# Kernel optimization log

Measured on AMD Instinct MI355X. Metric: run time of the kernel, lower is better.

## Reference

```python
import jax, jax.numpy as jnp
import numpy as np

IN_FEATURES = 4096
OUT_FEATURES = 4096
BINS = 65536
TOKENS = 8192


def setup_inputs() -> dict:
    key = jax.random.key(0)
    k_x, k_w, k_b, k_idx = jax.random.split(key, 4)
    bound = 1.0 / np.sqrt(OUT_FEATURES)
    x = jax.random.normal(k_x, (TOKENS, IN_FEATURES), dtype=jnp.float32)
    weight = jax.random.uniform(k_w, (BINS,), dtype=jnp.float32, minval=-bound, maxval=bound)
    bias = jax.random.uniform(k_b, (OUT_FEATURES,), dtype=jnp.float32, minval=-bound, maxval=bound)
    indices_hash = jax.random.randint(k_idx, (OUT_FEATURES * IN_FEATURES,), 0, BINS, dtype=jnp.int32)
    return {"x": x, "weight": weight, "bias": bias, "indices_hash": indices_hash}


def reference(x, weight, bias, indices_hash):
    # Reconstruct dense weight [out, in] by gathering from the shared bins.
    true_weight = jnp.take(weight, indices_hash, axis=0).reshape(OUT_FEATURES, IN_FEATURES)
    # F.linear: x @ W^T + b
    return jnp.einsum("ti,oi->to", x, true_weight) + bias
```

## Files before the change

kernel.cpp:

```cpp
#include <hip/hip_runtime.h>
#include <hip/hip_bf16.h>

#define TOKENS 8192
#define NOUT   4096
#define KIN    4096

typedef __attribute__((ext_vector_type(8))) short short8;
typedef __attribute__((ext_vector_type(4))) float f32x4;

__device__ __forceinline__ short f2bf(float f) {
  union { float f; unsigned u; } v; v.f = f;
  unsigned r = v.u + 0x7fffu + ((v.u >> 16) & 1u);
  return (short)(r >> 16);
}

__device__ __forceinline__ void async_copy16(const void* g, void* l) {
  __builtin_amdgcn_global_load_lds(
      (const __attribute__((address_space(1))) void*)g,
      (__attribute__((address_space(3))) void*)l, 16, 0, 0);
}

__global__ void pack_w_kernel(const int4* __restrict__ idx,
                              const float* __restrict__ w,
                              short8* __restrict__ wb) {
  size_t t = (size_t)blockIdx.x * blockDim.x + threadIdx.x;
  int4 a = idx[2 * t];
  int4 b = idx[2 * t + 1];
  short8 o;
  o[0] = f2bf(w[a.x]); o[1] = f2bf(w[a.y]);
  o[2] = f2bf(w[a.z]); o[3] = f2bf(w[a.w]);
  o[4] = f2bf(w[b.x]); o[5] = f2bf(w[b.y]);
  o[6] = f2bf(w[b.z]); o[7] = f2bf(w[b.w]);
  wb[t] = o;
}

__global__ void pack_x_kernel(const float4* __restrict__ x,
                              short8* __restrict__ xb) {
  size_t t = (size_t)blockIdx.x * blockDim.x + threadIdx.x;
  float4 a = x[2 * t];
  float4 b = x[2 * t + 1];
  short8 o;
  o[0] = f2bf(a.x); o[1] = f2bf(a.y); o[2] = f2bf(a.z); o[3] = f2bf(a.w);
  o[4] = f2bf(b.x); o[5] = f2bf(b.y); o[6] = f2bf(b.z); o[7] = f2bf(b.w);
  xb[t] = o;
}

#define BM 256
#define BN 256
#define BK 64
#define NT    (KIN / BK)
#define NITER (NT / 2)

#define BARX()  __builtin_amdgcn_s_barrier()
#define FENCE() __builtin_amdgcn_sched_barrier(0)
#define WAITVM(N) asm volatile("s_waitcnt vmcnt(" #N ")" ::: "memory")

__global__ __launch_bounds__(512, 2) void gemm_kernel(const short* __restrict__ A,
                                                      const short* __restrict__ B,
                                                      const float* __restrict__ bias,
                                                      float* __restrict__ C) {
  __shared__ short As[2][BM * BK];
  __shared__ short Bs[2][BN * BK];

  const int tid  = threadIdx.x;
  const int lane = tid & 63;
  const int wave = tid >> 6;
  const int wr = wave >> 2;
  const int wc = wave & 3;

  const int b   = blockIdx.x;
  const int swz = (b & 7) * 64 + (b >> 3);
  const int bm  = swz & 31;
  const int bn  = swz >> 5;

  const int srow = tid >> 3;
  const int sch  = ((tid & 7) ^ (srow & 7)) * 8;
  const short* aS = A + (size_t)(bm * 256 + srow) * KIN + sch;
  const short* bS = B + (size_t)(bn * 256 + srow) * KIN + sch;
  short* aD0 = &As[0][tid * 8];
  short* aD1 = &As[1][tid * 8];
  short* bD0 = &Bs[0][tid * 8];
  short* bD1 = &Bs[1][tid * 8];

#define STG_A(BUF, BLK, T) async_copy16(aS + (size_t)(BLK) * 64 * KIN + (size_t)(T) * 64, \
                                        ((BUF) ? aD1 : aD0) + (BLK) * 4096)
#define STG_B(BUF, BLK, T) async_copy16(bS + (size_t)(BLK) * 64 * KIN + (size_t)(T) * 64, \
                                        ((BUF) ? bD1 : bD0) + (BLK) * 4096)

  const int l15   = lane & 15;
  const int sw    = (l15 & 7) << 4;
  const int lanek = (lane >> 4) * 16;
  int csw[2];
  csw[0] = (0  + lanek) ^ sw;
  csw[1] = (64 + lanek) ^ sw;
  const int aBase = (wr * 128 + l15) * 128;
  const int bBase = (wc * 64  + l15) * 128;

  short8 af[4][2];
  short8 bfr[2][2][2];
  f32x4 acc[8][4] = {};

#define RD_A(BUF, MH) { const char* _p = (const char*)((BUF) ? As[1] : As[0]) + aBase + (MH) * 8192; \
  _Pragma("unroll") for (int mf = 0; mf < 4; ++mf) \
  _Pragma("unroll") for (int ks = 0; ks < 2; ++ks) \
    af[mf][ks] = *(const short8*)(_p + mf * 2048 + csw[ks]); }

#define RD_B(BUF, NH) { const char* _p = (const char*)((BUF) ? Bs[1] : Bs[0]) + bBase + (NH) * 4096; \
  _Pragma("unroll") for (int nf = 0; nf < 2; ++nf) \
  _Pragma("unroll") for (int ks = 0; ks < 2; ++ks) \
    bfr[NH][nf][ks] = *(const short8*)(_p + nf * 2048 + csw[ks]); }

#define MM(MH, NH) { __builtin_amdgcn_s_setprio(1); \
  _Pragma("unroll") for (int mf = 0; mf < 4; ++mf) \
  _Pragma("unroll") for (int nf = 0; nf < 2; ++nf) \
  _Pragma("unroll") for (int ks = 0; ks < 2; ++ks) \
    acc[(MH) * 4 + mf][(NH) * 2 + nf] = __builtin_amdgcn_mfma_f32_16x16x32_bf16( \
        af[mf][ks], bfr[NH][nf][ks], acc[(MH) * 4 + mf][(NH) * 2 + nf], 0, 0, 0); \
  __builtin_amdgcn_s_setprio(0); }

  STG_A(0, 0, 0); STG_A(0, 1, 0); STG_A(0, 2, 0); STG_A(0, 3, 0);
  STG_B(0, 0, 0); STG_B(0, 1, 0); STG_B(0, 2, 0); STG_B(0, 3, 0);
  STG_A(1, 0, 1); STG_A(1, 2, 1);
  WAITVM(2); FENCE(); BARX();

  for (int it = 0; it < NITER; ++it) {
    const int t1  = 2 * it + 1;
    const int tn0 = 2 * it + 2;
    const int tn1 = 2 * it + 3;
    const bool pf = (it < NITER - 1);

    RD_A(0, 0); RD_B(0, 0);
    STG_A(1, 1, t1); STG_A(1, 3, t1);
    BARX(); MM(0, 0); BARX();
    RD_B(0, 1);
    STG_B(1, 0, t1); STG_B(1, 1, t1);
    BARX(); MM(0, 1); BARX();
    RD_A(0, 1);
    STG_B(1, 2, t1); STG_B(1, 3, t1);
    BARX(); MM(1, 0); BARX();
    if (pf) { STG_A(0, 0, tn0); STG_A(0, 2, tn0); }
    BARX(); MM(1, 1);
    if (pf) { WAITVM(2); } else { WAITVM(0); }
    FENCE(); BARX();

    RD_A(1, 0); RD_B(1, 0);
    if (pf) { STG_A(0, 1, tn0); STG_A(0, 3, tn0); }
    BARX(); MM(0, 0); BARX();
    RD_B(1, 1);
    if (pf) { STG_B(0, 0, tn0); STG_B(0, 1, tn0); }
    BARX(); MM(0, 1); BARX();
    RD_A(1, 1);
    if (pf) { STG_B(0, 2, tn0); STG_B(0, 3, tn0); }
    BARX(); MM(1, 0); BARX();
    if (pf) { STG_A(1, 0, tn1); STG_A(1, 2, tn1); }
    BARX(); MM(1, 1);
    WAITVM(2); FENCE(); BARX();
  }

  const int crow0 = bm * 256 + wr * 128 + (lane >> 4) * 4;
  const int ccol0 = bn * 256 + wc * 64 + l15;
  float bsv[4];
#pragma unroll
  for (int nf = 0; nf < 4; ++nf) bsv[nf] = bias[ccol0 + nf * 16];
#pragma unroll
  for (int mf = 0; mf < 8; ++mf) {
#pragma unroll
    for (int j = 0; j < 4; ++j) {
      float* cr = C + (size_t)(crow0 + mf * 16 + j) * NOUT;
#pragma unroll
      for (int nf = 0; nf < 4; ++nf)
        cr[ccol0 + nf * 16] = acc[mf][nf][j] + bsv[nf];
    }
  }
}

extern "C" void kernel_launch(void* const* d_in, const int* in_sizes, int n_in,
                              void* d_out, int out_size, void* d_ws, size_t ws_size,
                              hipStream_t stream) {
  const float* x      = (const float*)d_in[0];
  const float* weight = (const float*)d_in[1];
  const float* bias   = (const float*)d_in[2];
  const int*   idx    = (const int*)d_in[3];
  float* out = (float*)d_out;

  short* wb = (short*)d_ws;
  short* xb = (short*)((char*)d_ws + (size_t)NOUT * KIN * sizeof(short));

  pack_w_kernel<<<((size_t)NOUT * KIN) / (8 * 256), 256, 0, stream>>>(
      (const int4*)idx, weight, (short8*)wb);
  pack_x_kernel<<<((size_t)TOKENS * KIN) / (8 * 256), 256, 0, stream>>>(
      (const float4*)x, (short8*)xb);
  gemm_kernel<<<(TOKENS / BM) * (NOUT / BN), 512, 0, stream>>>(xb, wb, bias, out);
}
```

Measured before the change: 590.9 us.

## Reorder B tile layout into N-halves and deepen async prefetch schedule

Changes the shared-memory layout of the B tile so each wave's two N-halves come from separate 32-row groups, which lets the B tile be staged in half-tile chunks. The load schedule is reworked so B for the next buffer is prefetched a full phase earlier, with more outstanding async loads (vmcnt 6 instead of 2) to overlap global-to-LDS traffic with MFMA work. This costs more in-flight loads and a more intricate wait schedule, and an index mistake in the remapping would produce wrong results.

```diff
diff --git a/kernel.cpp b/kernel.cpp
--- a/kernel.cpp
+++ b/kernel.cpp
@@ -73,10 +73,10 @@
   const int bm  = swz & 31;
   const int bn  = swz >> 5;
 
-  const int srow = tid >> 3;
-  const int sch  = ((tid & 7) ^ (srow & 7)) * 8;
-  const short* aS = A + (size_t)(bm * 256 + srow) * KIN + sch;
-  const short* bS = B + (size_t)(bn * 256 + srow) * KIN + sch;
+  const int sch  = (((tid & 7) ^ ((tid >> 3) & 7)) * 8);
+  const short* aS = A + (size_t)(bm * 256 + (tid >> 3)) * KIN + sch;
+  const int rB0 = ((tid >> 8) << 6) + ((tid >> 3) & 31);
+  const short* bS = B + (size_t)(bn * 256 + rB0) * KIN + sch;
   short* aD0 = &As[0][tid * 8];
   short* aD1 = &As[1][tid * 8];
   short* bD0 = &Bs[0][tid * 8];
@@ -84,8 +84,8 @@
 
 #define STG_A(BUF, BLK, T) async_copy16(aS + (size_t)(BLK) * 64 * KIN + (size_t)(T) * 64, \
                                         ((BUF) ? aD1 : aD0) + (BLK) * 4096)
-#define STG_B(BUF, BLK, T) async_copy16(bS + (size_t)(BLK) * 64 * KIN + (size_t)(T) * 64, \
-                                        ((BUF) ? bD1 : bD0) + (BLK) * 4096)
+#define STG_B(BUF, H, P, T) async_copy16(bS + ((size_t)((P) * 128 + (H) * 32)) * KIN + (size_t)(T) * 64, \
+                                         ((BUF) ? bD1 : bD0) + ((H) * 2 + (P)) * 4096)
 
   const int l15   = lane & 15;
   const int sw    = (l15 & 7) << 4;
@@ -94,7 +94,7 @@
   csw[0] = (0  + lanek) ^ sw;
   csw[1] = (64 + lanek) ^ sw;
   const int aBase = (wr * 128 + l15) * 128;
-  const int bBase = (wc * 64  + l15) * 128;
+  const int bBase = (wc * 32 + l15) * 128;
 
   short8 af[4][2];
   short8 bfr[2][2][2];
@@ -105,7 +105,7 @@
   _Pragma("unroll") for (int ks = 0; ks < 2; ++ks) \
     af[mf][ks] = *(const short8*)(_p + mf * 2048 + csw[ks]); }
 
-#define RD_B(BUF, NH) { const char* _p = (const char*)((BUF) ? Bs[1] : Bs[0]) + bBase + (NH) * 4096; \
+#define RD_B(BUF, NH) { const char* _p = (const char*)((BUF) ? Bs[1] : Bs[0]) + bBase + (NH) * 16384; \
   _Pragma("unroll") for (int nf = 0; nf < 2; ++nf) \
   _Pragma("unroll") for (int ks = 0; ks < 2; ++ks) \
     bfr[NH][nf][ks] = *(const short8*)(_p + nf * 2048 + csw[ks]); }
@@ -118,10 +118,14 @@
         af[mf][ks], bfr[NH][nf][ks], acc[(MH) * 4 + mf][(NH) * 2 + nf], 0, 0, 0); \
   __builtin_amdgcn_s_setprio(0); }
 
-  STG_A(0, 0, 0); STG_A(0, 1, 0); STG_A(0, 2, 0); STG_A(0, 3, 0);
-  STG_B(0, 0, 0); STG_B(0, 1, 0); STG_B(0, 2, 0); STG_B(0, 3, 0);
+  STG_A(0, 0, 0); STG_A(0, 2, 0);
+  STG_B(0, 0, 0, 0); STG_B(0, 0, 1, 0);
+  STG_B(0, 1, 0, 0); STG_B(0, 1, 1, 0);
+  STG_A(0, 1, 0); STG_A(0, 3, 0);
   STG_A(1, 0, 1); STG_A(1, 2, 1);
-  WAITVM(2); FENCE(); BARX();
+  STG_B(1, 0, 0, 1); STG_B(1, 0, 1, 1);
+  STG_B(1, 1, 0, 1); STG_B(1, 1, 1, 1);
+  WAITVM(6); FENCE(); BARX();
 
   for (int it = 0; it < NITER; ++it) {
     const int t1  = 2 * it + 1;
@@ -133,28 +137,29 @@
     STG_A(1, 1, t1); STG_A(1, 3, t1);
     BARX(); MM(0, 0); BARX();
     RD_B(0, 1);
-    STG_B(1, 0, t1); STG_B(1, 1, t1);
+    if (pf) { STG_A(0, 0, tn0); STG_A(0, 2, tn0); }
     BARX(); MM(0, 1); BARX();
     RD_A(0, 1);
-    STG_B(1, 2, t1); STG_B(1, 3, t1);
+    if (pf) { STG_B(0, 0, 0, tn0); STG_B(0, 0, 1, tn0); }
     BARX(); MM(1, 0); BARX();
-    if (pf) { STG_A(0, 0, tn0); STG_A(0, 2, tn0); }
+    if (pf) { STG_B(0, 1, 0, tn0); STG_B(0, 1, 1, tn0); }
     BARX(); MM(1, 1);
-    if (pf) { WAITVM(2); } else { WAITVM(0); }
+    if (pf) { WAITVM(6); } else { WAITVM(0); }
     FENCE(); BARX();
 
     RD_A(1, 0); RD_B(1, 0);
     if (pf) { STG_A(0, 1, tn0); STG_A(0, 3, tn0); }
     BARX(); MM(0, 0); BARX();
     RD_B(1, 1);
-    if (pf) { STG_B(0, 0, tn0); STG_B(0, 1, tn0); }
+    if (pf) { STG_A(1, 0, tn1); STG_A(1, 2, tn1); }
     BARX(); MM(0, 1); BARX();
     RD_A(1, 1);
-    if (pf) { STG_B(0, 2, tn0); STG_B(0, 3, tn0); }
+    if (pf) { STG_B(1, 0, 0, tn1); STG_B(1, 0, 1, tn1); }
     BARX(); MM(1, 0); BARX();
-    if (pf) { STG_A(1, 0, tn1); STG_A(1, 2, tn1); }
+    if (pf) { STG_B(1, 1, 0, tn1); STG_B(1, 1, 1, tn1); }
     BARX(); MM(1, 1);
-    WAITVM(2); FENCE(); BARX();
+    if (pf) { WAITVM(6); } else { WAITVM(0); }
+    FENCE(); BARX();
   }
 
   const int crow0 = bm * 256 + wr * 128 + (lane >> 4) * 4;
```

New measurement: 603.0 us. 1.02x slower.
